# Performance work log

Hardware: AMD Instinct MI355X
Metric: run time of the kernel (lower is better)

The kernel has to match this reference:

```python
import jax, jax.numpy as jnp
import numpy as np

HEADS = 8
DIM_HEADS = 64
M_DIM = 512
X_DIM = 512
MEM_NUM = 512
N = 16384
PERCENT = 0.25
LAY_NUMBER = 2       # outer refinement iterations
CROSS_LAYERS = 2     # layers inside M_cross_layers
EPS = 1e-5


def setup_inputs() -> dict:
    key = jax.random.key(0)
    ks = jax.random.split(key, 8)
    data = jax.random.normal(ks[0], (N, X_DIM), dtype=jnp.float32)
    Memory = jax.random.normal(ks[1], (MEM_NUM, M_DIM), dtype=jnp.float32)
    # to_kv: Linear(X_dim, 2*kv_dim, bias=False); kv_dim = heads*dim_heads
    Wkv = jax.random.normal(ks[2], (X_DIM, 2 * HEADS * DIM_HEADS), dtype=jnp.float32) * 0.02
    # per cross layer: to_q (no bias) and mutl_heads (with bias)
    Wq = jax.random.normal(ks[3], (CROSS_LAYERS, M_DIM, HEADS * DIM_HEADS), dtype=jnp.float32) * 0.02
    Wm = jax.random.normal(ks[4], (CROSS_LAYERS, HEADS * DIM_HEADS, M_DIM), dtype=jnp.float32) * 0.02
    bm = jnp.zeros((CROSS_LAYERS, M_DIM), dtype=jnp.float32)
    return {"data": data, "Memory": Memory, "Wkv": Wkv, "Wq": Wq, "Wm": Wm, "bm": bm, "istest": 0}


def _layer_norm(x):
    # F.layer_norm over last dim, no affine params
    mu = jnp.mean(x, axis=-1, keepdims=True)
    var = jnp.var(x, axis=-1, keepdims=True)
    return (x - mu) * jax.lax.rsqrt(var + EPS)


def _cross_layer(M, X, Wkv, Wq_l, Wm_l, bm_l):
    # cross_att + residual + layernorm (SublayerConnection); FFN is dead code in source
    q = (M @ Wq_l).reshape(MEM_NUM, HEADS, DIM_HEADS).transpose(1, 0, 2)      # [h, m, dh]
    kv = X @ Wkv                                                              # [n, 2*h*dh]
    k, v = jnp.split(kv, 2, axis=-1)
    k = k.reshape(-1, HEADS, DIM_HEADS).transpose(1, 0, 2)                    # [h, n, dh]
    v = v.reshape(-1, HEADS, DIM_HEADS).transpose(1, 0, 2)
    sim = jnp.einsum('hid,hjd->hij', q, k) * (DIM_HEADS ** -0.5)              # [h, m, n]
    att = jax.nn.softmax(sim, axis=-1)
    o = jnp.einsum('hij,hjd->hid', att, v)                                    # [h, m, dh]
    o = o.transpose(1, 0, 2).reshape(MEM_NUM, HEADS * DIM_HEADS)
    out = o @ Wm_l + bm_l                                                     # [m, M_dim]
    return _layer_norm(out + M)


def _cross_layers(M, X, Wkv, Wq, Wm, bm):
    for l in range(CROSS_LAYERS):
        M = _cross_layer(M, X, Wkv, Wq[l], Wm[l], bm[l])
    return M


def _calucate_sim(data, M):
    # per-sample landmark similarity: max scaled dot product against memory rows
    logits = (data @ M.T) * (DIM_HEADS ** -0.5)   # [N, mem]
    return jnp.max(logits, axis=-1)               # [N]


def _calucate_emb(data, M):
    logits = (data @ M.T) * (DIM_HEADS ** -0.5)   # [N, mem]
    logp = jax.nn.log_softmax(logits, axis=-1)
    p = jnp.exp(logp)
    out_ebs = p @ M                               # soft memory readout [N, M_dim]
    result_loss = -jnp.mean(jnp.max(logp, axis=-1))
    lse = jax.scipy.special.logsumexp(logits, axis=-1)
    zloss = jnp.mean(lse ** 2)                    # router-style z-loss
    return out_ebs, result_loss, zloss


def _select(data, sim_M, k):
    _, top_idx = jax.lax.top_k(sim_M, k)
    X = jnp.zeros_like(data)
    return X.at[top_idx].set(data[top_idx])


def reference(data, Memory, Wkv, Wq, Wm, bm, istest):
    M = Memory
    sim_M = _calucate_sim(data, M)
    percent_count = int(data.shape[0] * PERCENT)
    if not istest:
        X = _select(data, sim_M, percent_count)
        for _ in range(LAY_NUMBER):
            M = _cross_layers(M, X, Wkv, Wq, Wm, bm)
            sim_M = _calucate_sim(data, M)
            X = _select(data, sim_M, percent_count)
    out_ebs, result_loss, zloss = _calucate_emb(data, M)
    return (sim_M, out_ebs, result_loss, zloss)
```

## Files before the change

### kernel.cpp

```cpp
#include <hip/hip_runtime.h>
#include <cstdint>

#define N_DATA 16384
#define DIM 512
#define MEM 512
#define KSEL 4096
#define NH 8
#define DH 64
#define KVDIM 1024
#define SCALE 0.125f
#define ZCNT 12288.0f
#define LN_EPS 1e-5f
#define NSPLIT 4
#define ROWS_SP (KSEL / NSPLIT)

typedef unsigned short u16;
using short8 = __attribute__((ext_vector_type(8))) short;
using f32x4  = __attribute__((ext_vector_type(4))) float;

__device__ __forceinline__ unsigned fenc(float x) {
    unsigned u = __float_as_uint(x);
    return (u & 0x80000000u) ? ~u : (u | 0x80000000u);
}
__device__ __forceinline__ u16 f2bf(float x) {
    unsigned u = __float_as_uint(x);
    u += 0x7fffu + ((u >> 16) & 1u);
    return (u16)(u >> 16);
}
__device__ __forceinline__ float bf2f(u16 h) { return __uint_as_float(((unsigned)h) << 16); }

__device__ __forceinline__ float waveSum(float v) {
#pragma unroll
    for (int o = 32; o > 0; o >>= 1) v += __shfl_down(v, o, 64);
    return v;
}
__device__ float blockSum(float v) {
    __shared__ float sh[4];
    __syncthreads();
    v = waveSum(v);
    if ((threadIdx.x & 63) == 0) sh[threadIdx.x >> 6] = v;
    __syncthreads();
    if (threadIdx.x == 0) { float s = sh[0]; for (int i = 1; i < 4; ++i) s += sh[i]; sh[0] = s; }
    __syncthreads();
    return sh[0];
}

template<int ROWS, int NW, bool GATHER>
__device__ __forceinline__ void stage_tile(const u16* __restrict__ src, int ld, int k0,
                                           int row0, const int* __restrict__ gidx,
                                           u16* lds, int wave)
{
    constexpr int NI = ROWS / 16;
    const int lane = threadIdx.x & 63;
#pragma unroll
    for (int i = wave; i < NI; i += NW) {
        const int ch = i * 64 + lane;
        const int r = ch >> 2, cc = ch & 3;
        int rg = row0 + r;
        if (GATHER) rg = gidx[rg];
        const u16* g = src + (long)rg * ld + k0 + cc * 8;
        u16* l = lds + i * 512;
        __builtin_amdgcn_global_load_lds((const __attribute__((address_space(1))) void*)g,
                                         (__attribute__((address_space(3))) void*)l,
                                         16, 0, 0);
    }
}

template<int WM, int WN, bool GATHER, int EPI, bool BIAS>
__global__ __launch_bounds__(WM * WN * 64)
void mfma_gemm(const u16* __restrict__ A, const u16* __restrict__ B,
               const float* __restrict__ bias, const int* __restrict__ gidx,
               void* __restrict__ Cv, unsigned* __restrict__ simenc,
               u16* __restrict__ vTo,
               int K, int lda, int ldb, int ldc,
               long zsA, long zsB, long zsC, int zdiv, long zsplitC, float alpha)
{
    constexpr int BM = WM * 64, BN = WN * 64, NW = WM * WN;
    __shared__ __align__(16) u16 As[BM * 32];
    __shared__ __align__(16) u16 Bs[BN * 32];

    const int t = threadIdx.x;
    const int wave = t >> 6, lane = t & 63;
    const int wr = wave / WN, wc = wave % WN;
    const int l15 = lane & 15, l4 = lane >> 4;
    const int bm0 = blockIdx.x * BM, bn0 = blockIdx.y * BN;
    const int zs = (int)blockIdx.z % zdiv;
    const int zh = (int)blockIdx.z / zdiv;
    A += (long)zh * zsA;
    B += (long)zh * zsB;

    f32x4 acc[4][4];
#pragma unroll
    for (int i = 0; i < 4; ++i)
#pragma unroll
        for (int j = 0; j < 4; ++j)
#pragma unroll
            for (int r = 0; r < 4; ++r) acc[i][j][r] = 0.f;

    const int Kd = K / zdiv;
    const int kbeg = zs * Kd;
    for (int k0 = kbeg; k0 < kbeg + Kd; k0 += 32) {
        stage_tile<BM, NW, GATHER>(A, lda, k0, bm0, gidx, As, wave);
        stage_tile<BN, NW, false>(B, ldb, k0, bn0, nullptr, Bs, wave);
        __syncthreads();
        short8 a[4], b[4];
#pragma unroll
        for (int fm = 0; fm < 4; ++fm)
            a[fm] = *(const short8*)(As + (wr * 64 + fm * 16 + l15) * 32 + l4 * 8);
#pragma unroll
        for (int fn = 0; fn < 4; ++fn)
            b[fn] = *(const short8*)(Bs + (wc * 64 + fn * 16 + l15) * 32 + l4 * 8);
#pragma unroll
        for (int fm = 0; fm < 4; ++fm)
#pragma unroll
            for (int fn = 0; fn < 4; ++fn)
                acc[fm][fn] = __builtin_amdgcn_mfma_f32_16x16x32_bf16(a[fm], b[fn], acc[fm][fn], 0, 0, 0);
        __syncthreads();
    }

    if (EPI == 2) {
#pragma unroll
        for (int fm = 0; fm < 4; ++fm)
#pragma unroll
            for (int r = 0; r < 4; ++r) {
                float mx = acc[fm][0][r];
#pragma unroll
                for (int fn = 1; fn < 4; ++fn) mx = fmaxf(mx, acc[fm][fn][r]);
#pragma unroll
                for (int o = 8; o >= 1; o >>= 1) mx = fmaxf(mx, __shfl_xor(mx, o, 64));
                if (l15 == 0) {
                    const int row = bm0 + wr * 64 + fm * 16 + l4 * 4 + r;
                    atomicMax(simenc + row, fenc(alpha * mx));
                }
            }
    } else if (EPI == 0) {
        float* C = (float*)Cv + (long)zh * zsC + (long)zs * zsplitC;
#pragma unroll
        for (int fm = 0; fm < 4; ++fm)
#pragma unroll
            for (int fn = 0; fn < 4; ++fn)
#pragma unroll
                for (int r = 0; r < 4; ++r) {
                    const int row = bm0 + wr * 64 + fm * 16 + l4 * 4 + r;
                    const int col = bn0 + wc * 64 + fn * 16 + l15;
                    float v = alpha * acc[fm][fn][r];
                    if (BIAS) v += bias[col];
                    C[(long)row * ldc + col] = v;
                }
    } else if (EPI == 1) {
        u16* C = (u16*)Cv + (long)zh * zsC + (long)zs * zsplitC;
#pragma unroll
        for (int fm = 0; fm < 4; ++fm)
#pragma unroll
            for (int fn = 0; fn < 4; ++fn)
#pragma unroll
                for (int r = 0; r < 4; ++r) {
                    const int row = bm0 + wr * 64 + fm * 16 + l4 * 4 + r;
                    const int col = bn0 + wc * 64 + fn * 16 + l15;
                    float v = alpha * acc[fm][fn][r];
                    if (BIAS) v += bias[col];
                    C[(long)row * ldc + col] = f2bf(v);
                }
    } else {
        if (bn0 < 512) {
            u16* C = (u16*)Cv;
#pragma unroll
            for (int fm = 0; fm < 4; ++fm)
#pragma unroll
                for (int fn = 0; fn < 4; ++fn)
#pragma unroll
                    for (int r = 0; r < 4; ++r) {
                        const int row = bm0 + wr * 64 + fm * 16 + l4 * 4 + r;
                        const int col = bn0 + wc * 64 + fn * 16 + l15;
                        C[(long)row * ldc + col] = f2bf(alpha * acc[fm][fn][r]);
                    }
        } else {
#pragma unroll
            for (int fm = 0; fm < 4; ++fm)
#pragma unroll
                for (int fn = 0; fn < 4; ++fn) {
                    const int d = bn0 + wc * 64 + fn * 16 + l15 - 512;
                    const int row0 = bm0 + wr * 64 + fm * 16 + l4 * 4;
                    ushort4 pw;
                    pw.x = f2bf(alpha * acc[fm][fn][0]);
                    pw.y = f2bf(alpha * acc[fm][fn][1]);
                    pw.z = f2bf(alpha * acc[fm][fn][2]);
                    pw.w = f2bf(alpha * acc[fm][fn][3]);
                    *(ushort4*)(vTo + (long)d * 4096 + row0) = pw;
                }
        }
    }
}

__global__ __launch_bounds__(512)
void mfma_gemm_sm(const u16* __restrict__ A, const u16* __restrict__ B,
                  u16* __restrict__ Obf, float* __restrict__ simf,
                  float* __restrict__ lse, float* __restrict__ mlp, float alpha)
{
    __shared__ __align__(16) u16 As[64 * 32];
    __shared__ __align__(16) u16 Bs[512 * 32];
    const int t = threadIdx.x, wave = t >> 6, lane = t & 63;
    const int wc = wave;
    const int l15 = lane & 15, l4 = lane >> 4;
    const int bm0 = blockIdx.x * 64;

    f32x4 acc[4][4];
#pragma unroll
    for (int i = 0; i < 4; ++i)
#pragma unroll
        for (int j = 0; j < 4; ++j)
#pragma unroll
            for (int r = 0; r < 4; ++r) acc[i][j][r] = 0.f;

    for (int k0 = 0; k0 < 512; k0 += 32) {
        stage_tile<64, 8, false>(A, 512, k0, bm0, nullptr, As, wave);
        stage_tile<512, 8, false>(B, 512, k0, 0, nullptr, Bs, wave);
        __syncthreads();
        short8 a[4], b[4];
#pragma unroll
        for (int fm = 0; fm < 4; ++fm)
            a[fm] = *(const short8*)(As + (fm * 16 + l15) * 32 + l4 * 8);
#pragma unroll
        for (int fn = 0; fn < 4; ++fn)
            b[fn] = *(const short8*)(Bs + (wc * 64 + fn * 16 + l15) * 32 + l4 * 8);
#pragma unroll
        for (int fm = 0; fm < 4; ++fm)
#pragma unroll
            for (int fn = 0; fn < 4; ++fn)
                acc[fm][fn] = __builtin_amdgcn_mfma_f32_16x16x32_bf16(a[fm], b[fn], acc[fm][fn], 0, 0, 0);
        __syncthreads();
    }

    float* red  = (float*)As;
    float* rowv = (float*)Bs;

#pragma unroll
    for (int fm = 0; fm < 4; ++fm)
#pragma unroll
        for (int r = 0; r < 4; ++r) {
            float mx = alpha * acc[fm][0][r];
#pragma unroll
            for (int fn = 1; fn < 4; ++fn) mx = fmaxf(mx, alpha * acc[fm][fn][r]);
#pragma unroll
            for (int o = 1; o <= 8; o <<= 1) mx = fmaxf(mx, __shfl_xor(mx, o, 64));
            if (l15 == 0) red[(fm * 16 + l4 * 4 + r) * 8 + wc] = mx;
        }
    __syncthreads();
    if (t < 64) {
        float mx = red[t * 8];
#pragma unroll
        for (int j = 1; j < 8; ++j) mx = fmaxf(mx, red[t * 8 + j]);
        rowv[t] = mx;
    }
    __syncthreads();
#pragma unroll
    for (int fm = 0; fm < 4; ++fm)
#pragma unroll
        for (int r = 0; r < 4; ++r) {
            const int rl = fm * 16 + l4 * 4 + r;
            const float m = rowv[rl];
            float s = 0.f;
#pragma unroll
            for (int fn = 0; fn < 4; ++fn) s += __expf(alpha * acc[fm][fn][r] - m);
#pragma unroll
            for (int o = 1; o <= 8; o <<= 1) s += __shfl_xor(s, o, 64);
            if (l15 == 0) red[rl * 8 + wc] = s;
        }
    __syncthreads();
    if (t < 64) {
        float s = 0.f;
#pragma unroll
        for (int j = 0; j < 8; ++j) s += red[t * 8 + j];
        const float m = rowv[t];
        const float l = m + __logf(s);
        const int gr = bm0 + t;
        simf[gr] = m; lse[gr] = l; mlp[gr] = m - l;
        rowv[64 + t] = l;
    }
    __syncthreads();
#pragma unroll
    for (int fm = 0; fm < 4; ++fm)
#pragma unroll
        for (int r = 0; r < 4; ++r) {
            const int rl = fm * 16 + l4 * 4 + r;
            const float l = rowv[64 + rl];
#pragma unroll
            for (int fn = 0; fn < 4; ++fn) {
                const int col = wc * 64 + fn * 16 + l15;
                Obf[(long)(bm0 + rl) * 512 + col] = f2bf(__expf(alpha * acc[fm][fn][r] - l));
            }
        }
}

__global__ __launch_bounds__(512)
void wmln(const u16* __restrict__ A, const u16* __restrict__ BT,
          const float* __restrict__ bias, const float* __restrict__ Min,
          float* __restrict__ Mout, u16* __restrict__ Mbf,
          unsigned* __restrict__ simz, u16* __restrict__ MTout)
{
    __shared__ __align__(16) u16 As[16 * 32];
    __shared__ __align__(16) u16 Bs[512 * 32];
    __shared__ float red[16][8], red2[16][8], rowv[32];
    const int t = threadIdx.x, wave = t >> 6, lane = t & 63;
    const int wc = wave;
    const int l15 = lane & 15, l4 = lane >> 4;
    const int bm0 = blockIdx.x * 16;

    simz[blockIdx.x * 512 + t] = 0u;

    f32x4 acc[4];
#pragma unroll
    for (int fn = 0; fn < 4; ++fn)
#pragma unroll
        for (int r = 0; r < 4; ++r) acc[fn][r] = 0.f;

    for (int k0 = 0; k0 < 512; k0 += 32) {
        stage_tile<16, 8, false>(A, 512, k0, bm0, nullptr, As, wave);
        stage_tile<512, 8, false>(BT, 512, k0, 0, nullptr, Bs, wave);
        __syncthreads();
        const short8 a = *(const short8*)(As + l15 * 32 + l4 * 8);
#pragma unroll
        for (int fn = 0; fn < 4; ++fn) {
            const short8 b = *(const short8*)(Bs + (wc * 64 + fn * 16 + l15) * 32 + l4 * 8);
            acc[fn] = __builtin_amdgcn_mfma_f32_16x16x32_bf16(a, b, acc[fn], 0, 0, 0);
        }
        __syncthreads();
    }

    float v[4][4];
#pragma unroll
    for (int fn = 0; fn < 4; ++fn) {
        const int col = wc * 64 + fn * 16 + l15;
        const float bi = bias[col];
#pragma unroll
        for (int r = 0; r < 4; ++r) {
            const int row = bm0 + l4 * 4 + r;
            v[fn][r] = acc[fn][r] + bi + Min[(long)row * 512 + col];
        }
    }
#pragma unroll
    for (int r = 0; r < 4; ++r) {
        float s = 0.f, s2 = 0.f;
#pragma unroll
        for (int fn = 0; fn < 4; ++fn) { const float x = v[fn][r]; s += x; s2 += x * x; }
#pragma unroll
        for (int o = 1; o <= 8; o <<= 1) { s += __shfl_xor(s, o, 64); s2 += __shfl_xor(s2, o, 64); }
        if (l15 == 0) { red[l4 * 4 + r][wc] = s; red2[l4 * 4 + r][wc] = s2; }
    }
    __syncthreads();
    if (t < 16) {
        float s = 0.f, s2 = 0.f;
#pragma unroll
        for (int j = 0; j < 8; ++j) { s += red[t][j]; s2 += red2[t][j]; }
        const float mu = s * (1.f / 512.f);
        const float var = s2 * (1.f / 512.f) - mu * mu;
        rowv[t] = mu;
        rowv[16 + t] = rsqrtf(var + LN_EPS);
    }
    __syncthreads();
#pragma unroll
    for (int fn = 0; fn < 4; ++fn) {
        const int col = wc * 64 + fn * 16 + l15;
#pragma unroll
        for (int r = 0; r < 4; ++r) {
            const int rl = l4 * 4 + r;
            const float y = (v[fn][r] - rowv[rl]) * rowv[16 + rl];
            Mout[(long)(bm0 + rl) * 512 + col] = y;
            Mbf [(long)(bm0 + rl) * 512 + col] = f2bf(y);
            if (MTout) MTout[(long)col * 512 + (bm0 + rl)] = f2bf(y);
        }
    }
}

__global__ __launch_bounds__(256)
void flash_att(const u16* __restrict__ Mbf, const u16* __restrict__ WqT,
               const u16* __restrict__ KV, const u16* __restrict__ VT,
               float* __restrict__ oPart, float* __restrict__ mPart,
               float* __restrict__ lPart)
{
    __shared__ __align__(16) u16 Qs[64 * 64];
    __shared__ __align__(16) u16 Ks[2][64 * 64];
    __shared__ __align__(16) u16 Vs[2][64 * 64];
    __shared__ __align__(16) u16 Ps[4][16 * 72];

    const int qt = blockIdx.x, h = blockIdx.y, sp = blockIdx.z;
    const int t = threadIdx.x, wave = t >> 6, lane = t & 63;
    const int l15 = lane & 15, l4 = lane >> 4;

    const u16* Kg = KV + ((long)sp * ROWS_SP) * 1024 + h * 64;
    const u16* Vg = VT + ((long)h * 64) * 4096 + sp * ROWS_SP;

    auto stageKV = [&](int kt, int buf) {
        const u16* Kt = Kg + (long)(kt * 64) * 1024;
        const u16* Vt = Vg + kt * 64;
#pragma unroll
        for (int i = wave; i < 8; i += 4) {
            const int ch = i * 64 + lane, r = ch >> 3, s = ch & 7;
            __builtin_amdgcn_global_load_lds(
                (const __attribute__((address_space(1))) void*)(Kt + (long)r * 1024 + ((s ^ (r & 7)) * 8)),
                (__attribute__((address_space(3))) void*)(Ks[buf] + i * 512), 16, 0, 0);
        }
#pragma unroll
        for (int i = wave; i < 8; i += 4) {
            const int ch = i * 64 + lane, r = ch >> 3, s = ch & 7;
            __builtin_amdgcn_global_load_lds(
                (const __attribute__((address_space(1))) void*)(Vt + (long)r * 4096 + ((s ^ (r & 7)) * 8)),
                (__attribute__((address_space(3))) void*)(Vs[buf] + i * 512), 16, 0, 0);
        }
    };

    stageKV(0, 0);

    f32x4 accq[4];
#pragma unroll
    for (int fn = 0; fn < 4; ++fn)
#pragma unroll
        for (int r = 0; r < 4; ++r) accq[fn][r] = 0.f;
    {
        const u16* Ag = Mbf + (long)(qt * 64 + wave * 16 + l15) * 512 + l4 * 8;
        const u16* Bg = WqT + (long)(h * 64 + l15) * 512 + l4 * 8;
#pragma unroll 4
        for (int k0 = 0; k0 < 512; k0 += 32) {
            const short8 a = *(const short8*)(Ag + k0);
#pragma unroll
            for (int fn = 0; fn < 4; ++fn) {
                const short8 b = *(const short8*)(Bg + (long)fn * 16 * 512 + k0);
                accq[fn] = __builtin_amdgcn_mfma_f32_16x16x32_bf16(a, b, accq[fn], 0, 0, 0);
            }
        }
    }
#pragma unroll
    for (int fn = 0; fn < 4; ++fn)
#pragma unroll
        for (int r = 0; r < 4; ++r) {
            const int qrow = wave * 16 + l4 * 4 + r;
            const int col = fn * 16 + l15;
            Qs[qrow * 64 + (((col >> 3) ^ (qrow & 7)) << 3) + (col & 7)] = f2bf(accq[fn][r]);
        }
    __syncthreads();

    const int qr = wave * 16 + l15;
    short8 qf0 = *(const short8*)(Qs + qr * 64 + ((0 * 4 + l4) ^ (qr & 7)) * 8);
    short8 qf1 = *(const short8*)(Qs + qr * 64 + ((1 * 4 + l4) ^ (qr & 7)) * 8);

    float m = -3.0e38f, lsum = 0.f;
    f32x4 acc_o[4];
#pragma unroll
    for (int nf = 0; nf < 4; ++nf)
#pragma unroll
        for (int r = 0; r < 4; ++r) acc_o[nf][r] = 0.f;

    u16* myP = &Ps[wave][0];
    constexpr int NT = ROWS_SP / 64;
    int cur = 0;

    for (int kt = 0; kt < NT; ++kt) {
        if (kt + 1 < NT) stageKV(kt + 1, cur ^ 1);
        const u16* Kc = Ks[cur];
        const u16* Vc = Vs[cur];
        f32x4 acc_s[4];
#pragma unroll
        for (int mf = 0; mf < 4; ++mf) {
#pragma unroll
            for (int r = 0; r < 4; ++r) acc_s[mf][r] = 0.f;
            const int kr = mf * 16 + l15;
            const short8 ka0 = *(const short8*)(Kc + kr * 64 + ((0 * 4 + l4) ^ (kr & 7)) * 8);
            const short8 ka1 = *(const short8*)(Kc + kr * 64 + ((1 * 4 + l4) ^ (kr & 7)) * 8);
            acc_s[mf] = __builtin_amdgcn_mfma_f32_16x16x32_bf16(ka0, qf0, acc_s[mf], 0, 0, 0);
            acc_s[mf] = __builtin_amdgcn_mfma_f32_16x16x32_bf16(ka1, qf1, acc_s[mf], 0, 0, 0);
        }
        float sv[16];
#pragma unroll
        for (int mf = 0; mf < 4; ++mf)
#pragma unroll
            for (int r = 0; r < 4; ++r) sv[mf * 4 + r] = SCALE * acc_s[mf][r];
        float pm = sv[0];
#pragma unroll
        for (int j = 1; j < 16; ++j) pm = fmaxf(pm, sv[j]);
        pm = fmaxf(pm, __shfl_xor(pm, 16, 64));
        pm = fmaxf(pm, __shfl_xor(pm, 32, 64));
        const float mnew = fmaxf(m, pm);
        const float corr = __expf(m - mnew);
        float rs = 0.f;
#pragma unroll
        for (int j = 0; j < 16; ++j) { sv[j] = __expf(sv[j] - mnew); rs += sv[j]; }
        rs += __shfl_xor(rs, 16, 64);
        rs += __shfl_xor(rs, 32, 64);
        lsum = lsum * corr + rs;
        m = mnew;
        const float cf0 = __shfl(corr, l4 * 4 + 0, 64);
        const float cf1 = __shfl(corr, l4 * 4 + 1, 64);
        const float cf2 = __shfl(corr, l4 * 4 + 2, 64);
        const float cf3 = __shfl(corr, l4 * 4 + 3, 64);
#pragma unroll
        for (int nf = 0; nf < 4; ++nf) {
            acc_o[nf][0] *= cf0; acc_o[nf][1] *= cf1;
            acc_o[nf][2] *= cf2; acc_o[nf][3] *= cf3;
        }
#pragma unroll
        for (int mf = 0; mf < 4; ++mf) {
            ushort4 pw;
            pw.x = f2bf(sv[mf * 4 + 0]); pw.y = f2bf(sv[mf * 4 + 1]);
            pw.z = f2bf(sv[mf * 4 + 2]); pw.w = f2bf(sv[mf * 4 + 3]);
            *(ushort4*)(myP + l15 * 72 + mf * 16 + l4 * 4) = pw;
        }
#pragma unroll
        for (int ks = 0; ks < 2; ++ks) {
            const short8 pa = *(const short8*)(myP + l15 * 72 + ks * 32 + l4 * 8);
#pragma unroll
            for (int nf = 0; nf < 4; ++nf) {
                const int dr = nf * 16 + l15;
                const short8 vb = *(const short8*)(Vc + dr * 64 + ((ks * 4 + l4) ^ (dr & 7)) * 8);
                acc_o[nf] = __builtin_amdgcn_mfma_f32_16x16x32_bf16(pa, vb, acc_o[nf], 0, 0, 0);
            }
        }
        __syncthreads();
        cur ^= 1;
    }

    float* ob = oPart + (((long)sp * NH + h) * 8 + qt) * 4096;
#pragma unroll
    for (int nf = 0; nf < 4; ++nf)
#pragma unroll
        for (int r = 0; r < 4; ++r)
            ob[(wave * 16 + l4 * 4 + r) * 64 + nf * 16 + l15] = acc_o[nf][r];
    if (lane < 16) {
        const int qi = wave * 16 + lane;
        mPart[((sp * NH + h) * 8 + qt) * 64 + qi] = m;
        lPart[((sp * NH + h) * 8 + qt) * 64 + qi] = lsum;
    }
}

__global__ __launch_bounds__(256)
void flash_combine(const float* __restrict__ oPart, const float* __restrict__ mPart,
                   const float* __restrict__ lPart, u16* __restrict__ o_bf)
{
    const int qt = blockIdx.x & 7, h = blockIdx.x >> 3;
    const int t = threadIdx.x;
    const int q = t >> 2, d0 = (t & 3) << 4;
    float mi[NSPLIT], li[NSPLIT];
#pragma unroll
    for (int sp = 0; sp < NSPLIT; ++sp) {
        const int sb = ((sp * NH + h) * 8 + qt) * 64 + q;
        mi[sp] = mPart[sb];
        li[sp] = lPart[sb];
    }
    float ms = 0.f;
#pragma unroll
    for (int sp = 0; sp < NSPLIT; ++sp) ms = fmaxf(ms, mi[sp]);
    float denom = ZCNT * __expf(-ms);
    float f[NSPLIT];
#pragma unroll
    for (int sp = 0; sp < NSPLIT; ++sp) { f[sp] = __expf(mi[sp] - ms); denom += li[sp] * f[sp]; }
    const float inv = 1.f / denom;
    float o[16];
#pragma unroll
    for (int j = 0; j < 16; ++j) o[j] = 0.f;
#pragma unroll
    for (int sp = 0; sp < NSPLIT; ++sp) {
        const float* ob = oPart + (((long)sp * NH + h) * 8 + qt) * 4096 + q * 64 + d0;
        const float fs = f[sp] * inv;
#pragma unroll
        for (int j = 0; j < 16; j += 4) {
            const float4 v = *(const float4*)(ob + j);
            o[j] += fs * v.x; o[j + 1] += fs * v.y; o[j + 2] += fs * v.z; o[j + 3] += fs * v.w;
        }
    }
    u16* op = o_bf + (qt * 64 + q) * 512 + h * 64 + d0;
#pragma unroll
    for (int j = 0; j < 16; j += 4) {
        ushort4 w4;
        w4.x = f2bf(o[j]); w4.y = f2bf(o[j + 1]); w4.z = f2bf(o[j + 2]); w4.w = f2bf(o[j + 3]);
        *(ushort4*)(op + j) = w4;
    }
}

#define PRO_DATA 8192
#define PRO_W4   1024
#define PRO_WKV  512
#define PRO_MEM  256
#define PRO_SIM  16
__global__ __launch_bounds__(256)
void prologue(const float* __restrict__ data, const float* __restrict__ Memory,
              const float* __restrict__ Wkv, const float* __restrict__ Wq,
              const float* __restrict__ Wm,
              u16* __restrict__ data_bf, u16* __restrict__ Mbf,
              u16* __restrict__ WkvT, u16* __restrict__ WqT, u16* __restrict__ WmT,
              unsigned* __restrict__ simenc)
{
    __shared__ float tile[32][33];
    const int bid = blockIdx.x, t = threadIdx.x;
    if (bid < PRO_DATA) {
        const int i = (bid * 256 + t) * 4;
        const float4 v = *(const float4*)(data + i);
        ushort4 o;
        o.x = f2bf(v.x); o.y = f2bf(v.y); o.z = f2bf(v.z); o.w = f2bf(v.w);
        *(ushort4*)(data_bf + i) = o;
        return;
    }
    int b2 = bid - PRO_DATA;
    const int tx = t & 31, ty = t >> 5;
    if (b2 < PRO_W4) {
        const int z = b2 >> 8, q = b2 & 255;
        const float* S = (z < 2) ? (Wq + (long)z * DIM * DIM) : (Wm + (long)(z - 2) * DIM * DIM);
        u16* D = (z < 2) ? (WqT + (long)z * DIM * DIM) : (WmT + (long)(z - 2) * DIM * DIM);
        const int c0 = (q & 15) * 32, r0 = (q >> 4) * 32;
#pragma unroll
        for (int j = 0; j < 32; j += 8)
            tile[ty + j][tx] = S[(long)(r0 + ty + j) * DIM + c0 + tx];
        __syncthreads();
#pragma unroll
        for (int j = 0; j < 32; j += 8)
            D[(long)(c0 + ty + j) * DIM + r0 + tx] = f2bf(tile[tx][ty + j]);
        return;
    }
    b2 -= PRO_W4;
    if (b2 < PRO_WKV) {
        const int c0 = (b2 & 31) * 32, r0 = (b2 >> 5) * 32;
#pragma unroll
        for (int j = 0; j < 32; j += 8)
            tile[ty + j][tx] = Wkv[(long)(r0 + ty + j) * KVDIM + c0 + tx];
        __syncthreads();
#pragma unroll
        for (int j = 0; j < 32; j += 8)
            WkvT[(long)(c0 + ty + j) * DIM + r0 + tx] = f2bf(tile[tx][ty + j]);
        return;
    }
    b2 -= PRO_WKV;
    if (b2 < PRO_MEM) {
        const int i = (b2 * 256 + t) * 4;
        const float4 v = *(const float4*)(Memory + i);
        ushort4 o;
        o.x = f2bf(v.x); o.y = f2bf(v.y); o.z = f2bf(v.z); o.w = f2bf(v.w);
        *(ushort4*)(Mbf + i) = o;
        return;
    }
    b2 -= PRO_MEM;
    {
        const int i = (b2 * 256 + t) * 4;
        uint4 z; z.x = z.y = z.z = z.w = 0u;
        *(uint4*)(simenc + i) = z;
    }
}

__device__ __forceinline__ unsigned scan1024_excl(unsigned v, unsigned* wsum)
{
    const int lane = threadIdx.x & 63, wv = threadIdx.x >> 6;
    __syncthreads();
    unsigned x = v;
#pragma unroll
    for (int o = 1; o < 64; o <<= 1) {
        unsigned y = __shfl_up(x, o, 64);
        if (lane >= o) x += y;
    }
    if (lane == 63) wsum[wv] = x;
    __syncthreads();
    if (threadIdx.x < 16) {
        unsigned w2 = wsum[threadIdx.x];
#pragma unroll
        for (int o = 1; o < 16; o <<= 1) {
            unsigned y = __shfl_up(w2, o, 64);
            if ((int)threadIdx.x >= o) w2 += y;
        }
        wsum[threadIdx.x] = w2;
    }
    __syncthreads();
    const unsigned off = (wv > 0) ? wsum[wv - 1] : 0u;
    return off + x - v;
}

#define SEL_T 1024
#define SEL_CH (N_DATA / SEL_T)
__global__ __launch_bounds__(SEL_T)
void select_topk(const unsigned* __restrict__ key, int* __restrict__ idxo, int k)
{
    __shared__ unsigned whist[16][256];
    __shared__ unsigned hist[256];
    __shared__ unsigned wsum[16];
    __shared__ unsigned sh_bin, sh_r;
    const int t = threadIdx.x;
    const int wv = t >> 6;
    const int base = t * SEL_CH;

    unsigned kreg[SEL_CH];
#pragma unroll
    for (int c = 0; c < SEL_CH; ++c) kreg[c] = key[base + c];

    unsigned prefix = 0, mask = 0;
    unsigned r = (unsigned)k;
    for (int p = 3; p >= 0; --p) {
        __syncthreads();
        for (int i = t; i < 16 * 256; i += SEL_T) ((unsigned*)whist)[i] = 0u;
        __syncthreads();
#pragma unroll
        for (int c = 0; c < SEL_CH; ++c) {
            const unsigned kv = kreg[c];
            if ((kv & mask) == prefix)
                atomicAdd(&whist[wv][(kv >> (p * 8)) & 255u], 1u);
        }
        __syncthreads();
        if (t < 256) {
            unsigned s = 0;
#pragma unroll
            for (int wq = 0; wq < 16; ++wq) s += whist[wq][t];
            hist[t] = s;
        }
        __syncthreads();
        if (t < 64) {
            const int b0 = 255 - 4 * t;
            const unsigned c = hist[b0] + hist[b0 - 1] + hist[b0 - 2] + hist[b0 - 3];
            unsigned x = c;
#pragma unroll
            for (int o = 1; o < 64; o <<= 1) {
                unsigned y = __shfl_up(x, o, 64);
                if (t >= o) x += y;
            }
            const unsigned pre = x - c;
            if (pre < r && r <= x) {
                unsigned cum = pre;
#pragma unroll
                for (int j = 0; j < 4; ++j) {
                    const int b = b0 - j;
                    cum += hist[b];
                    if (cum >= r) { sh_bin = (unsigned)b; sh_r = r - (cum - hist[b]); break; }
                }
            }
        }
        __syncthreads();
        prefix |= sh_bin << (p * 8);
        mask |= 255u << (p * 8);
        r = sh_r;
    }
    const unsigned thr = prefix;
    const unsigned ties = r;

    unsigned ceq = 0;
#pragma unroll
    for (int c = 0; c < SEL_CH; ++c) ceq += (kreg[c] == thr) ? 1u : 0u;
    const unsigned eqbase = scan1024_excl(ceq, wsum);
    unsigned eq = eqbase, csel = 0;
#pragma unroll
    for (int c = 0; c < SEL_CH; ++c) {
        const unsigned kv = kreg[c];
        bool s;
        if (kv == thr) { s = (eq < ties); ++eq; }
        else s = (kv > thr);
        csel += s ? 1u : 0u;
    }
    unsigned pos = scan1024_excl(csel, wsum);
    eq = eqbase;
#pragma unroll
    for (int c = 0; c < SEL_CH; ++c) {
        const unsigned kv = kreg[c];
        bool s;
        if (kv == thr) { s = (eq < ties); ++eq; }
        else s = (kv > thr);
        if (s) idxo[pos++] = base + c;
    }
}

__global__ __launch_bounds__(256)
void reduce_loss(const float* __restrict__ lse, const float* __restrict__ mlp,
                 float* __restrict__ o2)
{
    const int t = threadIdx.x;
    float s1 = 0.f, s2 = 0.f;
    for (int i = t; i < N_DATA; i += 256) { s1 += mlp[i]; float l = lse[i]; s2 += l * l; }
    s1 = blockSum(s1);
    s2 = blockSum(s2);
    if (t == 0) { o2[0] = -s1 * (1.f / N_DATA); o2[1] = s2 * (1.f / N_DATA); }
}

extern "C" void kernel_launch(void* const* d_in, const int* in_sizes, int n_in,
                              void* d_out, int out_size, void* d_ws, size_t ws_size,
                              hipStream_t stream)
{
    (void)in_sizes; (void)n_in; (void)out_size; (void)ws_size;
    const float* data   = (const float*)d_in[0];
    const float* Memory = (const float*)d_in[1];
    const float* Wkv    = (const float*)d_in[2];
    const float* Wq     = (const float*)d_in[3];
    const float* Wm     = (const float*)d_in[4];
    const float* bm     = (const float*)d_in[5];
    float* out = (float*)d_out;

    char* w = (char*)d_ws;
    unsigned* simenc = (unsigned*)(w + 0);
    int*   idx     = (int*)  (w + 65536);
    float* lse     = (float*)(w + 81920);
    float* mlp     = (float*)(w + 147456);
    float* Ma      = (float*)(w + 262144);
    float* Mb      = (float*)(w + 1310720);
    u16*   Mbf0    = (u16*)  (w + 2359296);
    u16*   MT_bf   = (u16*)  (w + 2883584);
    u16*   WqT_bf  = (u16*)  (w + 3407872);
    u16*   WmT_bf  = (u16*)  (w + 4456448);
    u16*   WkvT_bf = (u16*)  (w + 5505024);
    u16*   o_bf    = (u16*)  (w + 7077888);
    u16*   data_bf = (u16*)  (w + 8650752);
    u16*   kvsel_bf= (u16*)  (w + 25427968);
    u16*   vT_bf   = (u16*)  (w + 33816576);
    float* oPart   = (float*)(w + 38010880);
    float* mPart   = (float*)(w + 42205184);
    float* lPart   = (float*)(w + 42270720);
    u16*   logits_bf = (u16*)(w + 54788096);
    u16*   Mbfa    = (u16*)  (w + 88342528);
    u16*   Mbfb    = (u16*)  (w + 88866816);

    prologue<<<PRO_DATA + PRO_W4 + PRO_WKV + PRO_MEM + PRO_SIM, 256, 0, stream>>>(
        data, Memory, Wkv, Wq, Wm, data_bf, Mbf0, WkvT_bf, WqT_bf, WmT_bf, simenc);

    auto sim_select_kv = [&](const u16* Mrows_bf) {
        mfma_gemm<2, 2, false, 2, false><<<dim3(128, 4, 1), 256, 0, stream>>>(
            data_bf, Mrows_bf, nullptr, nullptr, nullptr, simenc, nullptr,
            DIM, DIM, DIM, 0, 0, 0, 0, 1, 0, SCALE);
        select_topk<<<1, SEL_T, 0, stream>>>(simenc, idx, KSEL);
        mfma_gemm<2, 2, true, 3, false><<<dim3(32, 8, 1), 256, 0, stream>>>(
            data_bf, WkvT_bf, nullptr, idx, kvsel_bf, nullptr, vT_bf,
            DIM, DIM, DIM, KVDIM, 0, 0, 0, 1, 0, 1.0f);
    };

    auto cross = [&](const float* Mcur, const u16* Mcur_bf, float* Mnext, u16* Mnext_bf,
                     int l, u16* MTout) {
        flash_att<<<dim3(8, NH, NSPLIT), 256, 0, stream>>>(
            Mcur_bf, WqT_bf + (long)l * DIM * DIM, kvsel_bf, vT_bf, oPart, mPart, lPart);
        flash_combine<<<64, 256, 0, stream>>>(oPart, mPart, lPart, o_bf);
        wmln<<<32, 512, 0, stream>>>(
            o_bf, WmT_bf + (long)l * DIM * DIM, bm + (long)l * DIM, Mcur,
            Mnext, Mnext_bf, simenc, MTout);
    };

    const float* Mcur = Memory;
    const u16*  curbf = Mbf0;
    float* Mnext = Ma;
    u16*   nextbf = Mbfa;
    sim_select_kv(curbf);
    for (int it = 0; it < 2; ++it) {
        for (int l = 0; l < 2; ++l) {
            const bool last = (it == 1 && l == 1);
            cross(Mcur, curbf, Mnext, nextbf, l, last ? MT_bf : nullptr);
            Mcur = Mnext; curbf = nextbf;
            Mnext = (Mcur == Ma) ? Mb : Ma;
            nextbf = (curbf == Mbfa) ? Mbfb : Mbfa;
        }
        if (it == 0) sim_select_kv(curbf);
    }

    mfma_gemm_sm<<<N_DATA / 64, 512, 0, stream>>>(
        data_bf, curbf, logits_bf, out, lse, mlp, SCALE);
    mfma_gemm<2, 2, false, 0, false><<<dim3(128, 4, 1), 256, 0, stream>>>(
        logits_bf, MT_bf, nullptr, nullptr, out + N_DATA, nullptr, nullptr,
        MEM, MEM, MEM, DIM, 0, 0, 0, 1, 0, 1.0f);
    reduce_loss<<<1, 256, 0, stream>>>(lse, mlp, out + N_DATA + (long)N_DATA * DIM);
}
```

Before: 381.3 us.

## Fold loss reduction into final GEMM and use wave-aggregated histogram in top-k

Removes the separate reduce_loss launch and has block (0,0) of the final readout GEMM do the loss reduction after its tile, saving one kernel launch. In select_topk, the first radix pass now uses a ballot-based clustered add directly into a single shared histogram, which cuts atomic contention when many keys share a top byte. Key loads are also vectorized to uint4. The fused reduction lengthens one block's tail, and the clustered loop may iterate many times when bins are diverse.

```diff
diff --git a/kernel.cpp b/kernel.cpp
--- a/kernel.cpp
+++ b/kernel.cpp
@@ -66,12 +66,14 @@
     }
 }
 
-template<int WM, int WN, bool GATHER, int EPI, bool BIAS>
+template<int WM, int WN, bool GATHER, int EPI, bool BIAS, bool LOSS>
 __global__ __launch_bounds__(WM * WN * 64)
 void mfma_gemm(const u16* __restrict__ A, const u16* __restrict__ B,
                const float* __restrict__ bias, const int* __restrict__ gidx,
                void* __restrict__ Cv, unsigned* __restrict__ simenc,
                u16* __restrict__ vTo,
+               const float* __restrict__ lseIn, const float* __restrict__ mlpIn,
+               float* __restrict__ o2,
                int K, int lda, int ldb, int ldc,
                long zsA, long zsB, long zsC, int zdiv, long zsplitC, float alpha)
 {
@@ -188,6 +190,20 @@
                     pw.w = f2bf(alpha * acc[fm][fn][3]);
                     *(ushort4*)(vTo + (long)d * 4096 + row0) = pw;
                 }
+        }
+    }
+
+    if (LOSS) {
+        if (blockIdx.x == 0 && blockIdx.y == 0) {
+            float s1 = 0.f, s2 = 0.f;
+            for (int i = t; i < N_DATA; i += WM * WN * 64) {
+                s1 += mlpIn[i];
+                const float l = lseIn[i];
+                s2 += l * l;
+            }
+            s1 = blockSum(s1);
+            s2 = blockSum(s2);
+            if (t == 0) { o2[0] = -s1 * (1.f / N_DATA); o2[1] = s2 * (1.f / N_DATA); }
         }
     }
 }
@@ -669,6 +685,20 @@
     return off + x - v;
 }
 
+__device__ __forceinline__ void clustered_add(unsigned* hist, unsigned bin)
+{
+    bool pending = true;
+    while (__any(pending)) {
+        const unsigned long long mk = __ballot(pending);
+        const int lead = (int)__ffsll(mk) - 1;
+        const unsigned lbin = (unsigned)__shfl((int)bin, lead, 64);
+        const unsigned long long same = __ballot(pending && (bin == lbin));
+        if ((int)(threadIdx.x & 63) == lead)
+            atomicAdd(&hist[lbin], (unsigned)__popcll(same));
+        if (bin == lbin) pending = false;
+    }
+}
+
 #define SEL_T 1024
 #define SEL_CH (N_DATA / SEL_T)
 __global__ __launch_bounds__(SEL_T)
@@ -683,27 +713,42 @@
     const int base = t * SEL_CH;
 
     unsigned kreg[SEL_CH];
-#pragma unroll
-    for (int c = 0; c < SEL_CH; ++c) kreg[c] = key[base + c];
+    {
+        const uint4* kp = (const uint4*)(key + base);
+#pragma unroll
+        for (int q = 0; q < SEL_CH / 4; ++q) {
+            const uint4 v = kp[q];
+            kreg[q * 4 + 0] = v.x; kreg[q * 4 + 1] = v.y;
+            kreg[q * 4 + 2] = v.z; kreg[q * 4 + 3] = v.w;
+        }
+    }
 
     unsigned prefix = 0, mask = 0;
     unsigned r = (unsigned)k;
     for (int p = 3; p >= 0; --p) {
         __syncthreads();
-        for (int i = t; i < 16 * 256; i += SEL_T) ((unsigned*)whist)[i] = 0u;
-        __syncthreads();
-#pragma unroll
-        for (int c = 0; c < SEL_CH; ++c) {
-            const unsigned kv = kreg[c];
-            if ((kv & mask) == prefix)
-                atomicAdd(&whist[wv][(kv >> (p * 8)) & 255u], 1u);
-        }
-        __syncthreads();
-        if (t < 256) {
-            unsigned s = 0;
-#pragma unroll
-            for (int wq = 0; wq < 16; ++wq) s += whist[wq][t];
-            hist[t] = s;
+        if (p == 3) {
+            if (t < 256) hist[t] = 0u;
+            __syncthreads();
+#pragma unroll
+            for (int c = 0; c < SEL_CH; ++c)
+                clustered_add(hist, kreg[c] >> 24);
+        } else {
+            for (int i = t; i < 16 * 256; i += SEL_T) ((unsigned*)whist)[i] = 0u;
+            __syncthreads();
+#pragma unroll
+            for (int c = 0; c < SEL_CH; ++c) {
+                const unsigned kv = kreg[c];
+                if ((kv & mask) == prefix)
+                    atomicAdd(&whist[wv][(kv >> (p * 8)) & 255u], 1u);
+            }
+            __syncthreads();
+            if (t < 256) {
+                unsigned s = 0;
+#pragma unroll
+                for (int wq = 0; wq < 16; ++wq) s += whist[wq][t];
+                hist[t] = s;
+            }
         }
         __syncthreads();
         if (t < 64) {
@@ -757,18 +802,6 @@
         else s = (kv > thr);
         if (s) idxo[pos++] = base + c;
     }
-}
-
-__global__ __launch_bounds__(256)
-void reduce_loss(const float* __restrict__ lse, const float* __restrict__ mlp,
-                 float* __restrict__ o2)
-{
-    const int t = threadIdx.x;
-    float s1 = 0.f, s2 = 0.f;
-    for (int i = t; i < N_DATA; i += 256) { s1 += mlp[i]; float l = lse[i]; s2 += l * l; }
-    s1 = blockSum(s1);
-    s2 = blockSum(s2);
-    if (t == 0) { o2[0] = -s1 * (1.f / N_DATA); o2[1] = s2 * (1.f / N_DATA); }
 }
 
 extern "C" void kernel_launch(void* const* d_in, const int* in_sizes, int n_in,
@@ -811,12 +844,14 @@
         data, Memory, Wkv, Wq, Wm, data_bf, Mbf0, WkvT_bf, WqT_bf, WmT_bf, simenc);
 
     auto sim_select_kv = [&](const u16* Mrows_bf) {
-        mfma_gemm<2, 2, false, 2, false><<<dim3(128, 4, 1), 256, 0, stream>>>(
+        mfma_gemm<2, 2, false, 2, false, false><<<dim3(128, 4, 1), 256, 0, stream>>>(
             data_bf, Mrows_bf, nullptr, nullptr, nullptr, simenc, nullptr,
+            nullptr, nullptr, nullptr,
             DIM, DIM, DIM, 0, 0, 0, 0, 1, 0, SCALE);
         select_topk<<<1, SEL_T, 0, stream>>>(simenc, idx, KSEL);
-        mfma_gemm<2, 2, true, 3, false><<<dim3(32, 8, 1), 256, 0, stream>>>(
+        mfma_gemm<2, 2, true, 3, false, false><<<dim3(32, 8, 1), 256, 0, stream>>>(
             data_bf, WkvT_bf, nullptr, idx, kvsel_bf, nullptr, vT_bf,
+            nullptr, nullptr, nullptr,
             DIM, DIM, DIM, KVDIM, 0, 0, 0, 1, 0, 1.0f);
     };
 
@@ -848,8 +883,8 @@
 
     mfma_gemm_sm<<<N_DATA / 64, 512, 0, stream>>>(
         data_bf, curbf, logits_bf, out, lse, mlp, SCALE);
-    mfma_gemm<2, 2, false, 0, false><<<dim3(128, 4, 1), 256, 0, stream>>>(
+    mfma_gemm<2, 2, false, 0, false, true><<<dim3(128, 4, 1), 256, 0, stream>>>(
         logits_bf, MT_bf, nullptr, nullptr, out + N_DATA, nullptr, nullptr,
+        lse, mlp, out + N_DATA + (long)N_DATA * DIM,
         MEM, MEM, MEM, DIM, 0, 0, 0, 1, 0, 1.0f);
-    reduce_loss<<<1, 256, 0, stream>>>(lse, mlp, out + N_DATA + (long)N_DATA * DIM);
-}
+}
```

After: 375.2 us (median of 2 runs). Within noise of the previous version (-1.6%).
